# Optimization experiments

Measured on AMD Instinct MI355X. Metric: run time of the kernel, lower is better.

The kernel has to match this reference:

```python
import jax, jax.numpy as jnp
import numpy as np
import math

HIDDEN = 32
N_NODES = 4096
N_EDGES = 8192
FEAT = HIDDEN * 16
# e3nn FullyConnectedTensorProduct instruction order: loop i_in1, i_in2, i_out
PATHS = [(l1, l2, l3) for l1 in range(4) for l2 in range(4) for l3 in range(4)
         if abs(l1 - l2) <= l3 <= l1 + l2 and (l1 + l2 + l3) % 2 == 0]
WEIGHT_NUMEL = len(PATHS) * HIDDEN * HIDDEN  # 23 * 1024 = 23552
_CNT = {l3: sum(1 for p in PATHS if p[2] == l3) for l3 in range(4)}
# path_weight: irrep_normalization='component', path_normalization='element'
PATH_W = {p: math.sqrt((2 * p[2] + 1) / (_CNT[p[2]] * HIDDEN)) for p in PATHS}


def _sh(xp, x, y, z):
    # e3nn-convention real spherical harmonics l=0..3, 'component' normalization.
    # Assumes unit-norm (x,y,z). xp is np or jnp.
    s3, s5, s7, s15 = math.sqrt(3.), math.sqrt(5.), math.sqrt(7.), math.sqrt(15.)
    c58, c38 = math.sqrt(5. / 8.), math.sqrt(3. / 8.)
    comps = [
        xp.ones_like(x),
        s3 * x, s3 * y, s3 * z,
        s5 * s3 * x * z, s5 * s3 * x * y, s5 * (y * y - 0.5 * (x * x + z * z)),
        s5 * s3 * y * z, s5 * (s3 / 2.) * (z * z - x * x),
        s7 * c58 * x * (3. * z * z - x * x), s7 * s15 * x * y * z,
        s7 * c38 * x * (5. * y * y - 1.), s7 * 0.5 * y * (5. * y * y - 3.),
        s7 * c38 * z * (5. * y * y - 1.), s7 * (s15 / 2.) * y * (z * z - x * x),
        s7 * c58 * z * (z * z - 3. * x * x),
    ]
    return xp.stack(comps, axis=-1)


def _wigner_tables():
    # Real-basis unit-Frobenius invariant tensors (e3nn wigner_3j up to sign),
    # computed as Gaunt integrals of the real SH over the sphere (exact quadrature:
    # integrand degree <= 9, Gauss-Legendre x uniform phi).
    nu, nphi = 16, 32
    u, wu = np.polynomial.legendre.leggauss(nu)
    phi = np.arange(nphi) * (2.0 * np.pi / nphi)
    uu = np.repeat(u, nphi)
    ww = np.repeat(wu, nphi) * (2.0 * np.pi / nphi)
    pp = np.tile(phi, nu)
    st = np.sqrt(np.maximum(1.0 - uu * uu, 0.0))
    Y = _sh(np, st * np.cos(pp), st * np.sin(pp), uu)  # [P,16]
    tabs = {}
    for key in set(PATHS):
        l1, l2, l3 = key
        C = np.einsum('p,pi,pj,pk->ijk', ww,
                      Y[:, l1 * l1:(l1 + 1) ** 2],
                      Y[:, l2 * l2:(l2 + 1) ** 2],
                      Y[:, l3 * l3:(l3 + 1) ** 2])
        tabs[key] = (C / np.linalg.norm(C)).astype(np.float32)
    return tabs


W3J = _wigner_tables()


def setup_inputs():
    key = jax.random.key(0)
    k1, k2, k3, k4, k5 = jax.random.split(key, 5)
    return {
        'node_features': jax.random.normal(k1, (N_NODES, FEAT), jnp.float32),
        'edge_index': jax.random.randint(k2, (2, N_EDGES), 0, N_NODES),
        'edge_vectors': jax.random.normal(k3, (N_EDGES, 3), jnp.float32),
        'w_weight': jax.random.uniform(k4, (WEIGHT_NUMEL, 1), jnp.float32, -1.0, 1.0),
        'w_bias': jax.random.uniform(k5, (WEIGHT_NUMEL,), jnp.float32, -1.0, 1.0),
    }


def reference(node_features, edge_index, edge_vectors, w_weight, w_bias):
    src, dst = edge_index[0], edge_index[1]
    N = node_features.shape[0]
    E = edge_vectors.shape[0]
    lengths = jnp.maximum(jnp.linalg.norm(edge_vectors, axis=-1, keepdims=True), 1e-8)
    unit = edge_vectors / lengths
    Y = _sh(jnp, unit[:, 0], unit[:, 1], unit[:, 2])            # [E,16]
    # weight_net: Linear(1, weight_numel)
    W = lengths * w_weight[:, 0][None, :] + w_bias[None, :]     # [E,23552]
    x_src = node_features[src]                                  # [E,512] gather
    acc = [jnp.zeros((E, HIDDEN, 2 * l + 1), node_features.dtype) for l in range(4)]
    for p_idx, (l1, l2, l3) in enumerate(PATHS):
        x1 = x_src[:, HIDDEN * l1 * l1: HIDDEN * (l1 + 1) ** 2].reshape(E, HIDDEN, 2 * l1 + 1)
        y2 = Y[:, l2 * l2:(l2 + 1) ** 2]                        # [E,2l2+1]
        C = jnp.asarray(W3J[(l1, l2, l3)])                      # [2l1+1,2l2+1,2l3+1]
        wp = W[:, p_idx * HIDDEN * HIDDEN:(p_idx + 1) * HIDDEN * HIDDEN].reshape(E, HIDDEN, HIDDEN)
        tmp = jnp.einsum('eui,ej,ijk->euk', x1, y2, C)
        acc[l3] = acc[l3] + PATH_W[(l1, l2, l3)] * jnp.einsum('euk,euw->ewk', tmp, wp)
    messages = jnp.concatenate([a.reshape(E, -1) for a in acc], axis=-1)  # [E,512]
    return jax.ops.segment_sum(messages, dst, num_segments=N)
```

## Files before the change

### kernel.cpp

```cpp
#include <hip/hip_runtime.h>
#include <math.h>

#define N_PATHS 23
#define HIDDEN  32
#define N_NODES 4096
#define N_EDGES 8192
#define FEAT    512
#define BLK     128
#define ZERO_BLOCKS 256

#define WAVE_SYNC() asm volatile("s_waitcnt lgkmcnt(0)" ::: "memory")

typedef __attribute__((ext_vector_type(8)))  short bf16x8;
typedef __attribute__((ext_vector_type(16))) float f32x16;

constexpr int cL1[N_PATHS] = {0,0,0,0, 1,1,1,1,1,1, 2,2,2,2,2,2,2, 3,3,3,3,3,3};
constexpr int cL2[N_PATHS] = {0,1,2,3, 0,1,1,2,2,3, 0,1,1,2,2,3,3, 0,1,2,2,3,3};
constexpr int cCOFF[N_PATHS]= {0,1,10,35,84,93,102,147,192,297,402,427,472,577,602,727,832,1077,1126,1231,1336,1581,1630};
constexpr int cL3P[N_PATHS] = {0,5,13,21, 1,4,7,11,15,19, 2,6,9,10,14,18,22, 3,8,12,16,17,20};
constexpr int cL3S[5] = {0,4,10,17,23};
constexpr int cOFF3[4] = {0,32,128,288};
__device__ const int CNT_L3[4] = {4,6,7,6};
__device__ const int D_L3[N_PATHS] = {0,1,2,3, 1,0,2,1,3,2, 2,1,3,0,2,1,3, 3,2,1,3,0,2};

constexpr int zOff(int G, int pi) {
    int off = 0;
    for (int q = cL3S[G]; q < pi; ++q) off += (2*cL1[cL3P[q]]+1)*(2*G+1);
    return off;
}

__device__ const double GLX8[8] = {
    -0.96028985649753623168, -0.79666647741362673959, -0.52553240991632898582, -0.18343464249564980494,
     0.18343464249564980494,  0.52553240991632898582,  0.79666647741362673959,  0.96028985649753623168};
__device__ const double GLW8[8] = {
     0.10122853629037625915,  0.22238103445337447054,  0.31370664587788728734,  0.36268378337836198297,
     0.36268378337836198297,  0.31370664587788728734,  0.22238103445337447054,  0.10122853629037625915};
__device__ const double COSP16[16] = {
  1.0,                     0.92387953251128675613,  0.70710678118654752440,  0.38268343236508977173,
  0.0,                    -0.38268343236508977173, -0.70710678118654752440, -0.92387953251128675613,
 -1.0,                    -0.92387953251128675613, -0.70710678118654752440, -0.38268343236508977173,
  0.0,                     0.38268343236508977173,  0.70710678118654752440,  0.92387953251128675613};
__device__ const double SINP16[16] = {
  0.0,                     0.38268343236508977173,  0.70710678118654752440,  0.92387953251128675613,
  1.0,                     0.92387953251128675613,  0.70710678118654752440,  0.38268343236508977173,
  0.0,                    -0.38268343236508977173, -0.70710678118654752440, -0.92387953251128675613,
 -1.0,                    -0.92387953251128675613, -0.70710678118654752440, -0.38268343236508977173};

__device__ inline void sh_f64(double x, double y, double z, double* Y) {
    const double s3 = 1.7320508075688772935, s5 = 2.2360679774997896964,
                 s7 = 2.6457513110645905905, s15 = 3.8729833462074168852;
    const double c58 = 0.79056941504209483300, c38 = 0.61237243569579452455;
    Y[0] = 1.0;
    Y[1] = s3*x;  Y[2] = s3*y;  Y[3] = s3*z;
    Y[4] = s5*s3*x*z;  Y[5] = s5*s3*x*y;
    Y[6] = s5*(y*y - 0.5*(x*x + z*z));
    Y[7] = s5*s3*y*z;  Y[8] = s5*(s3/2.0)*(z*z - x*x);
    Y[9] = s7*c58*x*(3.0*z*z - x*x);
    Y[10]= s7*s15*x*y*z;
    Y[11]= s7*c38*x*(5.0*y*y - 1.0);
    Y[12]= s7*0.5*y*(5.0*y*y - 3.0);
    Y[13]= s7*c38*z*(5.0*y*y - 1.0);
    Y[14]= s7*(s15/2.0)*y*(z*z - x*x);
    Y[15]= s7*c58*z*(z*z - 3.0*x*x);
}

__device__ inline void sh_f32(float x, float y, float z, float* Y) {
    const float s3 = 1.73205080757f, s5 = 2.23606797750f, s7 = 2.64575131106f, s15 = 3.87298334621f;
    const float c58 = 0.79056941504f, c38 = 0.61237243570f;
    Y[0] = 1.0f;
    Y[1] = s3*x;  Y[2] = s3*y;  Y[3] = s3*z;
    Y[4] = s15*x*z;  Y[5] = s15*x*y;
    Y[6] = s5*(y*y - 0.5f*(x*x + z*z));
    Y[7] = s15*y*z;  Y[8] = s5*(s3*0.5f)*(z*z - x*x);
    Y[9] = s7*c58*x*(3.0f*z*z - x*x);
    Y[10]= s7*s15*x*y*z;
    Y[11]= s7*c38*x*(5.0f*y*y - 1.0f);
    Y[12]= s7*0.5f*y*(5.0f*y*y - 3.0f);
    Y[13]= s7*c38*z*(5.0f*y*y - 1.0f);
    Y[14]= s7*(s15*0.5f)*y*(z*z - x*x);
    Y[15]= s7*c58*z*(z*z - 3.0f*x*x);
}

__device__ inline unsigned short bf16rne(float x) {
    unsigned int u = __float_as_uint(x);
    unsigned int r = (u + 0x7FFFu + ((u >> 16) & 1u)) >> 16;
    return (unsigned short)r;
}
__device__ inline float bf16f(unsigned short h) {
    return __uint_as_float(((unsigned int)h) << 16);
}

__global__ __launch_bounds__(512) void w3j_setup_kernel(
    const float* __restrict__ ww, const float* __restrict__ wb,
    float* __restrict__ g_w3j,
    unsigned short* __restrict__ Awhi, unsigned short* __restrict__ Awlo,
    unsigned short* __restrict__ Abhi, unsigned short* __restrict__ Ablo,
    float* __restrict__ out) {
    const int t = threadIdx.x;

    if (blockIdx.x >= N_PATHS) {
        const int b = blockIdx.x - N_PATHS;
        float4* o4 = (float4*)(out + (size_t)b * (N_NODES*FEAT/ZERO_BLOCKS));
#pragma unroll
        for (int r = 0; r < 4; ++r)
            o4[t + 512*r] = make_float4(0.f,0.f,0.f,0.f);
        return;
    }

    __shared__ float s_Yq[128][17];
    __shared__ float s_wq[128];
    __shared__ float s_part[256];
    __shared__ float red[256];
    __shared__ float s_scale;

    const int p = blockIdx.x;
    const int l1 = cL1[p], l2 = cL2[p];
    const int l3 = D_L3[p];
    const int d2 = 2*l2+1, d3 = 2*l3+1;
    const int csize = (2*l1+1)*d2*d3;
    const double step = 2.0*3.14159265358979323846/16.0;

#pragma unroll
    for (int r = 0; r < 2; ++r) {
        const int idx = t + 512*r;
        const int w = idx >> 5, u = idx & 31;
        const float vw = ww[p*1024 + u*32 + w];
        const float vb = wb[p*1024 + u*32 + w];
        const unsigned short hw = bf16rne(vw);
        const unsigned short hb = bf16rne(vb);
        const int o = p*1024 + w*32 + u;
        Awhi[o] = hw;  Awlo[o] = bf16rne(vw - bf16f(hw));
        Abhi[o] = hb;  Ablo[o] = bf16rne(vb - bf16f(hb));
    }

    if (t < 128) {
        const int iu = t >> 4, ip = t & 15;
        const double u = GLX8[iu];
        const double st = sqrt(fmax(1.0 - u*u, 0.0));
        double Y[16];
        sh_f64(st*COSP16[ip], st*SINP16[ip], u, Y);
#pragma unroll
        for (int i = 0; i < 16; ++i) s_Yq[t][i] = (float)Y[i];
        s_wq[t] = (float)(GLW8[iu] * step);
    }
    __syncthreads();

    const int entry0 = t >> 2, sub = t & 3;
#pragma unroll
    for (int pass = 0; pass < 2; ++pass) {
        const int entry = entry0 + pass*128;
        float acc = 0.f;
        if (entry < csize) {
            const int i = entry/(d2*d3); const int r = entry - i*(d2*d3);
            const int j = r/d3; const int k = r - j*d3;
            const int ai = l1*l1+i, bi = l2*l2+j, ci = l3*l3+k;
#pragma unroll 4
            for (int it = 0; it < 32; ++it) {
                const int q = it*4 + sub;
                acc = fmaf(s_wq[q] * s_Yq[q][ai] * s_Yq[q][bi], s_Yq[q][ci], acc);
            }
        }
        acc += __shfl_xor(acc, 1);
        acc += __shfl_xor(acc, 2);
        if (sub == 0 && entry < csize) s_part[entry] = acc;
    }
    __syncthreads();

    if (t < 256) { const float v = (t < csize) ? s_part[t] : 0.f; red[t] = v*v; }
    __syncthreads();
    for (int s = 128; s > 0; s >>= 1) {
        if (t < s) red[t] += red[t+s];
        __syncthreads();
    }
    if (t == 0) {
        const float pw = sqrtf((float)(2*l3+1) / ((float)CNT_L3[l3] * (float)HIDDEN));
        s_scale = pw / sqrtf(red[0]);
    }
    __syncthreads();
    if (t < csize) g_w3j[cCOFF[p] + t] = s_part[t] * s_scale;
}

template<int G, int P, int ZOFF>
__device__ __forceinline__ void do_zpath(
    int lane, const float* __restrict__ w3j, const float* sY, float* sz)
{
    constexpr int l1 = cL1[P], l2 = cL2[P];
    constexpr int d1 = 2*l1+1, d2 = 2*l2+1, d3 = 2*G+1;
    constexpr int zc = d1*d3;
#pragma unroll
    for (int base = 0; base < 4*zc; base += 64) {
        const int idx = base + lane;
        if (idx < 4*zc) {
            const int elz = idx / zc;
            const int r = idx - elz*zc;
            const int i = r / d3, k = r - i*d3;
            const float* Cp = w3j + cCOFF[P] + i*(d2*d3) + k;
            const float* Yp = sY + elz*16 + l2*l2;
            float acc = 0.f;
#pragma unroll
            for (int j = 0; j < d2; ++j) acc = fmaf(Yp[j], Cp[j*d3], acc);
            sz[4*ZOFF + elz*zc + r] = acc;
        }
    }
}

template<int G, int P, int ZOFF>
__device__ __forceinline__ void do_path(
    int lane, int el4, int u0, int bvaddr, int avaddr,
    const float (&xr0)[16], const float (&xr1)[16],
    const unsigned short* __restrict__ Awhi, const unsigned short* __restrict__ Awlo,
    const unsigned short* __restrict__ Abhi, const unsigned short* __restrict__ Ablo,
    const float* sz,
    unsigned short* sbh, unsigned short* sbl,
    f32x16 &Cw, f32x16 &Cb)
{
    constexpr int l1 = cL1[P];
    constexpr int d1 = 2*l1+1, d3 = 2*G+1;
    constexpr int zc = d1*d3;
    constexpr int xo = l1*l1;

    const unsigned short* pwh = Awhi + P*1024;
    const unsigned short* pwl = Awlo + P*1024;
    const unsigned short* pbh = Abhi + P*1024;
    const unsigned short* pbl = Ablo + P*1024;
    bf16x8 awh[2], awl[2], abh[2], abl[2];
#pragma unroll
    for (int kc = 0; kc < 2; ++kc) {
        awh[kc] = *(const bf16x8*)(pwh + avaddr + kc*16);
        awl[kc] = *(const bf16x8*)(pwl + avaddr + kc*16);
        abh[kc] = *(const bf16x8*)(pbh + avaddr + kc*16);
        abl[kc] = *(const bf16x8*)(pbl + avaddr + kc*16);
    }

    {
        const float* zr = sz + 4*ZOFF + el4*zc;
        unsigned short* bh = sbh + (el4*d3)*40 + 2*u0;
        unsigned short* bl = sbl + (el4*d3)*40 + 2*u0;
#pragma unroll
        for (int k = 0; k < d3; ++k) {
            float t0 = 0.f, t1 = 0.f;
#pragma unroll
            for (int i = 0; i < d1; ++i) {
                const float zz = zr[i*d3 + k];
                t0 = fmaf(xr0[xo+i], zz, t0);
                t1 = fmaf(xr1[xo+i], zz, t1);
            }
            const unsigned int b0 = __float_as_uint(t0);
            const unsigned int b1 = __float_as_uint(t1);
            const float l0 = t0 - __uint_as_float(b0 & 0xFFFF0000u);
            const float l1f = t1 - __uint_as_float(b1 & 0xFFFF0000u);
            *(unsigned int*)(bh + k*40) = (b0 >> 16) | (b1 & 0xFFFF0000u);
            *(unsigned int*)(bl + k*40) = (__float_as_uint(l0) >> 16) | (__float_as_uint(l1f) & 0xFFFF0000u);
        }
    }
    WAVE_SYNC();

#pragma unroll
    for (int kc = 0; kc < 2; ++kc) {
        const bf16x8 bh = *(const bf16x8*)(sbh + bvaddr + kc*16);
        const bf16x8 bl = *(const bf16x8*)(sbl + bvaddr + kc*16);
        Cw = __builtin_amdgcn_mfma_f32_32x32x16_bf16(awh[kc], bh, Cw, 0, 0, 0);
        Cb = __builtin_amdgcn_mfma_f32_32x32x16_bf16(abh[kc], bh, Cb, 0, 0, 0);
        Cw = __builtin_amdgcn_mfma_f32_32x32x16_bf16(awh[kc], bl, Cw, 0, 0, 0);
        Cb = __builtin_amdgcn_mfma_f32_32x32x16_bf16(abh[kc], bl, Cb, 0, 0, 0);
        Cw = __builtin_amdgcn_mfma_f32_32x32x16_bf16(awl[kc], bh, Cw, 0, 0, 0);
        Cb = __builtin_amdgcn_mfma_f32_32x32x16_bf16(abl[kc], bh, Cb, 0, 0, 0);
    }
    WAVE_SYNC();
}

template<int G>
__device__ __forceinline__ void do_group(
    int lane, int el4, int u0, int bvaddr, int avaddr,
    const float (&xr0)[16], const float (&xr1)[16],
    const float* __restrict__ w3j,
    const unsigned short* __restrict__ Awhi, const unsigned short* __restrict__ Awlo,
    const unsigned short* __restrict__ Abhi, const unsigned short* __restrict__ Ablo,
    const float* sY, float* sz,
    unsigned short* sbh, unsigned short* sbl,
    const float* slen, float* smsg)
{
    constexpr int d3 = 2*G+1;
    constexpr int s = cL3S[G];
    constexpr int n = cL3S[G+1] - cL3S[G];
    f32x16 Cw = (f32x16)(0.f), Cb = (f32x16)(0.f);

    do_zpath<G, cL3P[s+0], zOff(G,s+0)>(lane, w3j, sY, sz);
    do_zpath<G, cL3P[s+1], zOff(G,s+1)>(lane, w3j, sY, sz);
    do_zpath<G, cL3P[s+2], zOff(G,s+2)>(lane, w3j, sY, sz);
    do_zpath<G, cL3P[s+3], zOff(G,s+3)>(lane, w3j, sY, sz);
    if constexpr (n > 4) do_zpath<G, cL3P[s+4], zOff(G,s+4)>(lane, w3j, sY, sz);
    if constexpr (n > 5) do_zpath<G, cL3P[s+5], zOff(G,s+5)>(lane, w3j, sY, sz);
    if constexpr (n > 6) do_zpath<G, cL3P[s+6], zOff(G,s+6)>(lane, w3j, sY, sz);
    WAVE_SYNC();

    do_path<G, cL3P[s+0], zOff(G,s+0)>(lane,el4,u0,bvaddr,avaddr,xr0,xr1,Awhi,Awlo,Abhi,Ablo,sz,sbh,sbl,Cw,Cb);
    do_path<G, cL3P[s+1], zOff(G,s+1)>(lane,el4,u0,bvaddr,avaddr,xr0,xr1,Awhi,Awlo,Abhi,Ablo,sz,sbh,sbl,Cw,Cb);
    do_path<G, cL3P[s+2], zOff(G,s+2)>(lane,el4,u0,bvaddr,avaddr,xr0,xr1,Awhi,Awlo,Abhi,Ablo,sz,sbh,sbl,Cw,Cb);
    do_path<G, cL3P[s+3], zOff(G,s+3)>(lane,el4,u0,bvaddr,avaddr,xr0,xr1,Awhi,Awlo,Abhi,Ablo,sz,sbh,sbl,Cw,Cb);
    if constexpr (n > 4)
        do_path<G, cL3P[s+4], zOff(G,s+4)>(lane,el4,u0,bvaddr,avaddr,xr0,xr1,Awhi,Awlo,Abhi,Ablo,sz,sbh,sbl,Cw,Cb);
    if constexpr (n > 5)
        do_path<G, cL3P[s+5], zOff(G,s+5)>(lane,el4,u0,bvaddr,avaddr,xr0,xr1,Awhi,Awlo,Abhi,Ablo,sz,sbh,sbl,Cw,Cb);
    if constexpr (n > 6)
        do_path<G, cL3P[s+6], zOff(G,s+6)>(lane,el4,u0,bvaddr,avaddr,xr0,xr1,Awhi,Awlo,Abhi,Ablo,sz,sbh,sbl,Cw,Cb);

    const int col = lane & 31;
    if (col < 4*d3) {
        const int elc = col / d3, k = col - elc*d3;
        const float len = slen[elc];
        float* mp = smsg + elc*FEAT + cOFF3[G] + k;
#pragma unroll
        for (int reg = 0; reg < 16; ++reg) {
            const int w = (reg & 3) + 8*(reg >> 2) + 4*(lane >> 5);
            mp[w*d3] = fmaf(len, Cw[reg], Cb[reg]);
        }
    }
}

__global__ __launch_bounds__(BLK) void edge_kernel(
    const float* __restrict__ nf,
    const int*   __restrict__ eidx,
    const float* __restrict__ ev,
    const float* __restrict__ w3j,
    const unsigned short* __restrict__ Awhi,
    const unsigned short* __restrict__ Awlo,
    const unsigned short* __restrict__ Abhi,
    const unsigned short* __restrict__ Ablo,
    float*       __restrict__ out)
{
    __shared__ float s_zp[2][784];
    __shared__ float s_Y[2][64];
    __shared__ float s_len[2][4];
    __shared__ int   s_src[2][4];
    __shared__ int   s_dst[2][4];
    __shared__ __align__(16) unsigned short s_Bhi[2][1280];
    __shared__ __align__(16) unsigned short s_Blo[2][1280];
    __shared__ float s_msg[2][4*FEAT];

    const int t    = threadIdx.x;
    const int wave = t >> 6;
    const int lane = t & 63;
    const int el4  = lane >> 4;
    const int u0   = lane & 15;
    const int e0   = blockIdx.x * 8 + wave*4;
    const int bvaddr = (lane & 31)*40 + (lane >> 5)*8;
    const int avaddr = (lane & 31)*32 + (lane >> 5)*8;

    if (lane < 4) {
        const int e = e0 + lane;
        s_src[wave][lane] = eidx[e];
        s_dst[wave][lane] = eidx[N_EDGES + e];
        const float x = ev[e*3+0], y = ev[e*3+1], z = ev[e*3+2];
        const float len = sqrtf(x*x + y*y + z*z);
        const float lc = fmaxf(len, 1e-8f);
        s_len[wave][lane] = lc;
        float Yl[16];
        sh_f32(x/lc, y/lc, z/lc, Yl);
#pragma unroll
        for (int i = 0; i < 16; ++i) s_Y[wave][lane*16+i] = Yl[i];
    }
    WAVE_SYNC();

    float xr0[16], xr1[16];
    {
        const float* xrow = nf + (size_t)s_src[wave][el4]*FEAT;
        const int ua = 2*u0, ub = 2*u0 + 1;
        xr0[0] = xrow[ua];                 xr1[0] = xrow[ub];
#pragma unroll
        for (int i = 0; i < 3; ++i) { xr0[1+i] = xrow[32 + ua*3 + i];  xr1[1+i] = xrow[32 + ub*3 + i]; }
#pragma unroll
        for (int i = 0; i < 5; ++i) { xr0[4+i] = xrow[128 + ua*5 + i]; xr1[4+i] = xrow[128 + ub*5 + i]; }
#pragma unroll
        for (int i = 0; i < 7; ++i) { xr0[9+i] = xrow[288 + ua*7 + i]; xr1[9+i] = xrow[288 + ub*7 + i]; }
    }

    do_group<0>(lane,el4,u0,bvaddr,avaddr,xr0,xr1,w3j,Awhi,Awlo,Abhi,Ablo,
                s_Y[wave], s_zp[wave], s_Bhi[wave], s_Blo[wave], s_len[wave], s_msg[wave]);
    do_group<1>(lane,el4,u0,bvaddr,avaddr,xr0,xr1,w3j,Awhi,Awlo,Abhi,Ablo,
                s_Y[wave], s_zp[wave], s_Bhi[wave], s_Blo[wave], s_len[wave], s_msg[wave]);
    do_group<2>(lane,el4,u0,bvaddr,avaddr,xr0,xr1,w3j,Awhi,Awlo,Abhi,Ablo,
                s_Y[wave], s_zp[wave], s_Bhi[wave], s_Blo[wave], s_len[wave], s_msg[wave]);
    do_group<3>(lane,el4,u0,bvaddr,avaddr,xr0,xr1,w3j,Awhi,Awlo,Abhi,Ablo,
                s_Y[wave], s_zp[wave], s_Bhi[wave], s_Blo[wave], s_len[wave], s_msg[wave]);
    WAVE_SYNC();

    for (int i = lane; i < 4*FEAT; i += 64) {
        const int elc = i >> 9, m = i & 511;
        atomicAdd(&out[(size_t)s_dst[wave][elc]*FEAT + m], s_msg[wave][i]);
    }
}

extern "C" void kernel_launch(void* const* d_in, const int* in_sizes, int n_in,
                              void* d_out, int out_size, void* d_ws, size_t ws_size,
                              hipStream_t stream) {
    const float* nf   = (const float*)d_in[0];
    const int*   eidx = (const int*)  d_in[1];
    const float* ev   = (const float*)d_in[2];
    const float* ww   = (const float*)d_in[3];
    const float* wb   = (const float*)d_in[4];
    float* out = (float*)d_out;

    float* w3j = (float*)d_ws;
    unsigned short* Awhi = (unsigned short*)((char*)d_ws + 16384);
    unsigned short* Awlo = Awhi + N_PATHS*1024;
    unsigned short* Abhi = Awlo + N_PATHS*1024;
    unsigned short* Ablo = Abhi + N_PATHS*1024;

    w3j_setup_kernel<<<N_PATHS + ZERO_BLOCKS, 512, 0, stream>>>(
        ww, wb, w3j, Awhi, Awlo, Abhi, Ablo, out);
    edge_kernel<<<N_EDGES/8, BLK, 0, stream>>>(nf, eidx, ev, w3j, Awhi, Awlo, Abhi, Ablo, out);
}
```

Before: 122.2 us.

## Replace per-path template unrolling with runtime loops and stage source features in LDS

Swaps the fully template-unrolled per-path code for runtime loops driven by device lookup tables. This should shrink code size and register pressure. Source node features are now loaded coalesced into shared memory in an irrep-transposed layout instead of held in per-thread register arrays. The atomic scatter to the output moves into each l3 group, so the message buffer shrinks to one group. The cost is extra LDS traffic, table lookups, non-constexpr loop bounds inside the rewritten loops, and more LDS per block.

```diff
diff --git a/kernel.cpp b/kernel.cpp
--- a/kernel.cpp
+++ b/kernel.cpp
@@ -14,20 +14,20 @@
 typedef __attribute__((ext_vector_type(8)))  short bf16x8;
 typedef __attribute__((ext_vector_type(16))) float f32x16;
 
-constexpr int cL1[N_PATHS] = {0,0,0,0, 1,1,1,1,1,1, 2,2,2,2,2,2,2, 3,3,3,3,3,3};
-constexpr int cL2[N_PATHS] = {0,1,2,3, 0,1,1,2,2,3, 0,1,1,2,2,3,3, 0,1,2,2,3,3};
-constexpr int cCOFF[N_PATHS]= {0,1,10,35,84,93,102,147,192,297,402,427,472,577,602,727,832,1077,1126,1231,1336,1581,1630};
-constexpr int cL3P[N_PATHS] = {0,5,13,21, 1,4,7,11,15,19, 2,6,9,10,14,18,22, 3,8,12,16,17,20};
 constexpr int cL3S[5] = {0,4,10,17,23};
 constexpr int cOFF3[4] = {0,32,128,288};
 __device__ const int CNT_L3[4] = {4,6,7,6};
-__device__ const int D_L3[N_PATHS] = {0,1,2,3, 1,0,2,1,3,2, 2,1,3,0,2,1,3, 3,2,1,3,0,2};
-
-constexpr int zOff(int G, int pi) {
-    int off = 0;
-    for (int q = cL3S[G]; q < pi; ++q) off += (2*cL1[cL3P[q]]+1)*(2*G+1);
-    return off;
-}
+
+__device__ const int mPATH[N_PATHS] = {0,5,13,21, 1,4,7,11,15,19, 2,6,9,10,14,18,22, 3,8,12,16,17,20};
+__device__ const int mD1  [N_PATHS] = {1,3,5,7, 1,3,3,5,5,7, 1,3,3,5,5,7,7, 1,3,5,5,7,7};
+__device__ const int mXO  [N_PATHS] = {0,1,4,9, 0,1,1,4,4,9, 0,1,1,4,4,9,9, 0,1,4,4,9,9};
+__device__ const int mL2  [N_PATHS] = {0,1,2,3, 1,0,2,1,3,2, 2,1,3,0,2,1,3, 3,2,1,3,0,2};
+__device__ const int mCOFF[N_PATHS] = {0,93,577,1581, 1,84,147,427,727,1231, 10,102,297,402,602,1126,1630, 35,192,472,832,1077,1336};
+__device__ const int mZOFF[N_PATHS] = {0,1,4,9, 0,3,12,21,36,51, 0,5,20,35,60,85,120, 0,7,28,63,98,147};
+__device__ const int pL1[N_PATHS] = {0,0,0,0, 1,1,1,1,1,1, 2,2,2,2,2,2,2, 3,3,3,3,3,3};
+__device__ const int pL2[N_PATHS] = {0,1,2,3, 0,1,1,2,2,3, 0,1,1,2,2,3,3, 0,1,2,2,3,3};
+__device__ const int pCOFF[N_PATHS]= {0,1,10,35,84,93,102,147,192,297,402,427,472,577,602,727,832,1077,1126,1231,1336,1581,1630};
+__device__ const int pD_L3[N_PATHS] = {0,1,2,3, 1,0,2,1,3,2, 2,1,3,0,2,1,3, 3,2,1,3,0,2};
 
 __device__ const double GLX8[8] = {
     -0.96028985649753623168, -0.79666647741362673959, -0.52553240991632898582, -0.18343464249564980494,
@@ -114,8 +114,8 @@
     __shared__ float s_scale;
 
     const int p = blockIdx.x;
-    const int l1 = cL1[p], l2 = cL2[p];
-    const int l3 = D_L3[p];
+    const int l1 = pL1[p], l2 = pL2[p];
+    const int l3 = pD_L3[p];
     const int d2 = 2*l2+1, d3 = 2*l3+1;
     const int csize = (2*l1+1)*d2*d3;
     const double step = 2.0*3.14159265358979323846/16.0;
@@ -177,145 +177,139 @@
         s_scale = pw / sqrtf(red[0]);
     }
     __syncthreads();
-    if (t < csize) g_w3j[cCOFF[p] + t] = s_part[t] * s_scale;
-}
-
-template<int G, int P, int ZOFF>
-__device__ __forceinline__ void do_zpath(
-    int lane, const float* __restrict__ w3j, const float* sY, float* sz)
-{
-    constexpr int l1 = cL1[P], l2 = cL2[P];
-    constexpr int d1 = 2*l1+1, d2 = 2*l2+1, d3 = 2*G+1;
-    constexpr int zc = d1*d3;
-#pragma unroll
-    for (int base = 0; base < 4*zc; base += 64) {
-        const int idx = base + lane;
-        if (idx < 4*zc) {
-            const int elz = idx / zc;
-            const int r = idx - elz*zc;
-            const int i = r / d3, k = r - i*d3;
-            const float* Cp = w3j + cCOFF[P] + i*(d2*d3) + k;
-            const float* Yp = sY + elz*16 + l2*l2;
-            float acc = 0.f;
-#pragma unroll
-            for (int j = 0; j < d2; ++j) acc = fmaf(Yp[j], Cp[j*d3], acc);
-            sz[4*ZOFF + elz*zc + r] = acc;
-        }
-    }
-}
-
-template<int G, int P, int ZOFF>
-__device__ __forceinline__ void do_path(
-    int lane, int el4, int u0, int bvaddr, int avaddr,
-    const float (&xr0)[16], const float (&xr1)[16],
-    const unsigned short* __restrict__ Awhi, const unsigned short* __restrict__ Awlo,
-    const unsigned short* __restrict__ Abhi, const unsigned short* __restrict__ Ablo,
-    const float* sz,
-    unsigned short* sbh, unsigned short* sbl,
-    f32x16 &Cw, f32x16 &Cb)
-{
-    constexpr int l1 = cL1[P];
-    constexpr int d1 = 2*l1+1, d3 = 2*G+1;
-    constexpr int zc = d1*d3;
-    constexpr int xo = l1*l1;
-
-    const unsigned short* pwh = Awhi + P*1024;
-    const unsigned short* pwl = Awlo + P*1024;
-    const unsigned short* pbh = Abhi + P*1024;
-    const unsigned short* pbl = Ablo + P*1024;
-    bf16x8 awh[2], awl[2], abh[2], abl[2];
-#pragma unroll
-    for (int kc = 0; kc < 2; ++kc) {
-        awh[kc] = *(const bf16x8*)(pwh + avaddr + kc*16);
-        awl[kc] = *(const bf16x8*)(pwl + avaddr + kc*16);
-        abh[kc] = *(const bf16x8*)(pbh + avaddr + kc*16);
-        abl[kc] = *(const bf16x8*)(pbl + avaddr + kc*16);
-    }
-
-    {
-        const float* zr = sz + 4*ZOFF + el4*zc;
-        unsigned short* bh = sbh + (el4*d3)*40 + 2*u0;
-        unsigned short* bl = sbl + (el4*d3)*40 + 2*u0;
-#pragma unroll
-        for (int k = 0; k < d3; ++k) {
-            float t0 = 0.f, t1 = 0.f;
-#pragma unroll
-            for (int i = 0; i < d1; ++i) {
-                const float zz = zr[i*d3 + k];
-                t0 = fmaf(xr0[xo+i], zz, t0);
-                t1 = fmaf(xr1[xo+i], zz, t1);
-            }
-            const unsigned int b0 = __float_as_uint(t0);
-            const unsigned int b1 = __float_as_uint(t1);
-            const float l0 = t0 - __uint_as_float(b0 & 0xFFFF0000u);
-            const float l1f = t1 - __uint_as_float(b1 & 0xFFFF0000u);
-            *(unsigned int*)(bh + k*40) = (b0 >> 16) | (b1 & 0xFFFF0000u);
-            *(unsigned int*)(bl + k*40) = (__float_as_uint(l0) >> 16) | (__float_as_uint(l1f) & 0xFFFF0000u);
-        }
-    }
-    WAVE_SYNC();
-
-#pragma unroll
-    for (int kc = 0; kc < 2; ++kc) {
-        const bf16x8 bh = *(const bf16x8*)(sbh + bvaddr + kc*16);
-        const bf16x8 bl = *(const bf16x8*)(sbl + bvaddr + kc*16);
-        Cw = __builtin_amdgcn_mfma_f32_32x32x16_bf16(awh[kc], bh, Cw, 0, 0, 0);
-        Cb = __builtin_amdgcn_mfma_f32_32x32x16_bf16(abh[kc], bh, Cb, 0, 0, 0);
-        Cw = __builtin_amdgcn_mfma_f32_32x32x16_bf16(awh[kc], bl, Cw, 0, 0, 0);
-        Cb = __builtin_amdgcn_mfma_f32_32x32x16_bf16(abh[kc], bl, Cb, 0, 0, 0);
-        Cw = __builtin_amdgcn_mfma_f32_32x32x16_bf16(awl[kc], bh, Cw, 0, 0, 0);
-        Cb = __builtin_amdgcn_mfma_f32_32x32x16_bf16(abl[kc], bh, Cb, 0, 0, 0);
-    }
-    WAVE_SYNC();
+    if (t < csize) g_w3j[pCOFF[p] + t] = s_part[t] * s_scale;
 }
 
 template<int G>
 __device__ __forceinline__ void do_group(
     int lane, int el4, int u0, int bvaddr, int avaddr,
-    const float (&xr0)[16], const float (&xr1)[16],
     const float* __restrict__ w3j,
     const unsigned short* __restrict__ Awhi, const unsigned short* __restrict__ Awlo,
     const unsigned short* __restrict__ Abhi, const unsigned short* __restrict__ Ablo,
-    const float* sY, float* sz,
+    const float* sY, const float* sx, float* sz,
     unsigned short* sbh, unsigned short* sbl,
-    const float* slen, float* smsg)
+    const float* slen, const int* sdst, float* smsg, float* __restrict__ out)
 {
     constexpr int d3 = 2*G+1;
-    constexpr int s = cL3S[G];
-    constexpr int n = cL3S[G+1] - cL3S[G];
+    constexpr int s0 = cL3S[G];
+    constexpr int n  = cL3S[G+1] - cL3S[G];
     f32x16 Cw = (f32x16)(0.f), Cb = (f32x16)(0.f);
 
-    do_zpath<G, cL3P[s+0], zOff(G,s+0)>(lane, w3j, sY, sz);
-    do_zpath<G, cL3P[s+1], zOff(G,s+1)>(lane, w3j, sY, sz);
-    do_zpath<G, cL3P[s+2], zOff(G,s+2)>(lane, w3j, sY, sz);
-    do_zpath<G, cL3P[s+3], zOff(G,s+3)>(lane, w3j, sY, sz);
-    if constexpr (n > 4) do_zpath<G, cL3P[s+4], zOff(G,s+4)>(lane, w3j, sY, sz);
-    if constexpr (n > 5) do_zpath<G, cL3P[s+5], zOff(G,s+5)>(lane, w3j, sY, sz);
-    if constexpr (n > 6) do_zpath<G, cL3P[s+6], zOff(G,s+6)>(lane, w3j, sY, sz);
+#pragma unroll 1
+    for (int j = 0; j < n; ++j) {
+        const int s   = s0 + j;
+        const int l2  = mL2[s];
+        const int d2  = 2*l2 + 1;
+        const int d1  = mD1[s];
+        const int zc  = d1*d3;
+        const int cof = mCOFF[s];
+        const int zo4 = 4*mZOFF[s];
+        if (lane < zc) {
+            const int i = lane / d3;
+            const int k = lane - i*d3;
+            const float* Cp = w3j + cof + i*(d2*d3) + k;
+#pragma unroll
+            for (int el = 0; el < 4; ++el) {
+                const float* Yp = sY + el*16 + l2*l2;
+                float acc = 0.f;
+                for (int jj = 0; jj < d2; ++jj) acc = fmaf(Yp[jj], Cp[jj*d3], acc);
+                sz[zo4 + el*zc + lane] = acc;
+            }
+        }
+    }
     WAVE_SYNC();
 
-    do_path<G, cL3P[s+0], zOff(G,s+0)>(lane,el4,u0,bvaddr,avaddr,xr0,xr1,Awhi,Awlo,Abhi,Ablo,sz,sbh,sbl,Cw,Cb);
-    do_path<G, cL3P[s+1], zOff(G,s+1)>(lane,el4,u0,bvaddr,avaddr,xr0,xr1,Awhi,Awlo,Abhi,Ablo,sz,sbh,sbl,Cw,Cb);
-    do_path<G, cL3P[s+2], zOff(G,s+2)>(lane,el4,u0,bvaddr,avaddr,xr0,xr1,Awhi,Awlo,Abhi,Ablo,sz,sbh,sbl,Cw,Cb);
-    do_path<G, cL3P[s+3], zOff(G,s+3)>(lane,el4,u0,bvaddr,avaddr,xr0,xr1,Awhi,Awlo,Abhi,Ablo,sz,sbh,sbl,Cw,Cb);
-    if constexpr (n > 4)
-        do_path<G, cL3P[s+4], zOff(G,s+4)>(lane,el4,u0,bvaddr,avaddr,xr0,xr1,Awhi,Awlo,Abhi,Ablo,sz,sbh,sbl,Cw,Cb);
-    if constexpr (n > 5)
-        do_path<G, cL3P[s+5], zOff(G,s+5)>(lane,el4,u0,bvaddr,avaddr,xr0,xr1,Awhi,Awlo,Abhi,Ablo,sz,sbh,sbl,Cw,Cb);
-    if constexpr (n > 6)
-        do_path<G, cL3P[s+6], zOff(G,s+6)>(lane,el4,u0,bvaddr,avaddr,xr0,xr1,Awhi,Awlo,Abhi,Ablo,sz,sbh,sbl,Cw,Cb);
-
+#pragma unroll 1
+    for (int j = 0; j < n; ++j) {
+        const int s    = s0 + j;
+        const int Poff = mPATH[s] << 10;
+        const int d1   = mD1[s];
+        const int xo   = mXO[s];
+        const int zc   = d1*d3;
+        const int zo4  = 4*mZOFF[s];
+
+        bf16x8 awh[2], awl[2], abh[2], abl[2];
+#pragma unroll
+        for (int kc = 0; kc < 2; ++kc) {
+            awh[kc] = *(const bf16x8*)(Awhi + Poff + avaddr + kc*16);
+            awl[kc] = *(const bf16x8*)(Awlo + Poff + avaddr + kc*16);
+            abh[kc] = *(const bf16x8*)(Abhi + Poff + avaddr + kc*16);
+            abl[kc] = *(const bf16x8*)(Ablo + Poff + avaddr + kc*16);
+        }
+
+        {
+            const float* zr = sz + zo4 + el4*zc;
+            const float* xp = sx + el4*512 + xo*32 + 2*u0;
+            float tk0[d3], tk1[d3];
+#pragma unroll
+            for (int k = 0; k < d3; ++k) { tk0[k] = 0.f; tk1[k] = 0.f; }
+            float2 xv = *(const float2*)(xp);
+            float zrow[d3];
+#pragma unroll
+            for (int k = 0; k < d3; ++k) zrow[k] = zr[k];
+            for (int i = 0; i < d1; ++i) {
+                const int ip = (i+1 < d1) ? (i+1) : i;
+                const float2 xn = *(const float2*)(xp + ip*32);
+                float zn[d3];
+#pragma unroll
+                for (int k = 0; k < d3; ++k) zn[k] = zr[ip*d3 + k];
+#pragma unroll
+                for (int k = 0; k < d3; ++k) {
+                    tk0[k] = fmaf(xv.x, zrow[k], tk0[k]);
+                    tk1[k] = fmaf(xv.y, zrow[k], tk1[k]);
+                }
+                xv = xn;
+#pragma unroll
+                for (int k = 0; k < d3; ++k) zrow[k] = zn[k];
+            }
+            unsigned short* bh = sbh + (el4*d3)*40 + 2*u0;
+            unsigned short* bl = sbl + (el4*d3)*40 + 2*u0;
+#pragma unroll
+            for (int k = 0; k < d3; ++k) {
+                const unsigned int b0 = __float_as_uint(tk0[k]);
+                const unsigned int b1 = __float_as_uint(tk1[k]);
+                const float l0  = tk0[k] - __uint_as_float(b0 & 0xFFFF0000u);
+                const float l1f = tk1[k] - __uint_as_float(b1 & 0xFFFF0000u);
+                *(unsigned int*)(bh + k*40) = (b0 >> 16) | (b1 & 0xFFFF0000u);
+                *(unsigned int*)(bl + k*40) = (__float_as_uint(l0) >> 16) | (__float_as_uint(l1f) & 0xFFFF0000u);
+            }
+        }
+        WAVE_SYNC();
+
+#pragma unroll
+        for (int kc = 0; kc < 2; ++kc) {
+            const bf16x8 bh = *(const bf16x8*)(sbh + bvaddr + kc*16);
+            const bf16x8 bl = *(const bf16x8*)(sbl + bvaddr + kc*16);
+            Cw = __builtin_amdgcn_mfma_f32_32x32x16_bf16(awh[kc], bh, Cw, 0, 0, 0);
+            Cb = __builtin_amdgcn_mfma_f32_32x32x16_bf16(abh[kc], bh, Cb, 0, 0, 0);
+            Cw = __builtin_amdgcn_mfma_f32_32x32x16_bf16(awh[kc], bl, Cw, 0, 0, 0);
+            Cb = __builtin_amdgcn_mfma_f32_32x32x16_bf16(abh[kc], bl, Cb, 0, 0, 0);
+            Cw = __builtin_amdgcn_mfma_f32_32x32x16_bf16(awl[kc], bh, Cw, 0, 0, 0);
+            Cb = __builtin_amdgcn_mfma_f32_32x32x16_bf16(abl[kc], bh, Cb, 0, 0, 0);
+        }
+        WAVE_SYNC();
+    }
+
+    constexpr int gsz = 32*d3;
     const int col = lane & 31;
     if (col < 4*d3) {
         const int elc = col / d3, k = col - elc*d3;
         const float len = slen[elc];
-        float* mp = smsg + elc*FEAT + cOFF3[G] + k;
+        float* mp = smsg + elc*gsz + k;
 #pragma unroll
         for (int reg = 0; reg < 16; ++reg) {
             const int w = (reg & 3) + 8*(reg >> 2) + 4*(lane >> 5);
             mp[w*d3] = fmaf(len, Cw[reg], Cb[reg]);
         }
     }
+    WAVE_SYNC();
+
+    for (int i2 = lane; i2 < 4*gsz; i2 += 64) {
+        const int el = i2 / gsz;
+        const int m  = i2 - el*gsz;
+        atomicAdd(&out[(size_t)sdst[el]*FEAT + cOFF3[G] + m], smsg[el*gsz + m]);
+    }
+    WAVE_SYNC();
 }
 
 __global__ __launch_bounds__(BLK) void edge_kernel(
@@ -336,7 +330,8 @@
     __shared__ int   s_dst[2][4];
     __shared__ __align__(16) unsigned short s_Bhi[2][1280];
     __shared__ __align__(16) unsigned short s_Blo[2][1280];
-    __shared__ float s_msg[2][4*FEAT];
+    __shared__ float s_msg[2][896];
+    __shared__ float s_x[2][2048];
 
     const int t    = threadIdx.x;
     const int wave = t >> 6;
@@ -362,33 +357,46 @@
     }
     WAVE_SYNC();
 
-    float xr0[16], xr1[16];
     {
-        const float* xrow = nf + (size_t)s_src[wave][el4]*FEAT;
-        const int ua = 2*u0, ub = 2*u0 + 1;
-        xr0[0] = xrow[ua];                 xr1[0] = xrow[ub];
-#pragma unroll
-        for (int i = 0; i < 3; ++i) { xr0[1+i] = xrow[32 + ua*3 + i];  xr1[1+i] = xrow[32 + ub*3 + i]; }
-#pragma unroll
-        for (int i = 0; i < 5; ++i) { xr0[4+i] = xrow[128 + ua*5 + i]; xr1[4+i] = xrow[128 + ub*5 + i]; }
-#pragma unroll
-        for (int i = 0; i < 7; ++i) { xr0[9+i] = xrow[288 + ua*7 + i]; xr1[9+i] = xrow[288 + ub*7 + i]; }
-    }
-
-    do_group<0>(lane,el4,u0,bvaddr,avaddr,xr0,xr1,w3j,Awhi,Awlo,Abhi,Ablo,
-                s_Y[wave], s_zp[wave], s_Bhi[wave], s_Blo[wave], s_len[wave], s_msg[wave]);
-    do_group<1>(lane,el4,u0,bvaddr,avaddr,xr0,xr1,w3j,Awhi,Awlo,Abhi,Ablo,
-                s_Y[wave], s_zp[wave], s_Bhi[wave], s_Blo[wave], s_len[wave], s_msg[wave]);
-    do_group<2>(lane,el4,u0,bvaddr,avaddr,xr0,xr1,w3j,Awhi,Awlo,Abhi,Ablo,
-                s_Y[wave], s_zp[wave], s_Bhi[wave], s_Blo[wave], s_len[wave], s_msg[wave]);
-    do_group<3>(lane,el4,u0,bvaddr,avaddr,xr0,xr1,w3j,Awhi,Awlo,Abhi,Ablo,
-                s_Y[wave], s_zp[wave], s_Bhi[wave], s_Blo[wave], s_len[wave], s_msg[wave]);
+        float* sx = s_x[wave];
+#pragma unroll
+        for (int idx = lane; idx < 4*32; idx += 64) {
+            const int el = idx >> 5, m = idx & 31;
+            sx[el*512 + m] = nf[(size_t)s_src[wave][el]*FEAT + m];
+        }
+#pragma unroll
+        for (int idx = lane; idx < 4*96; idx += 64) {
+            const int el = idx/96, m = idx - el*96;
+            const int u = m/3, i = m - 3*u;
+            sx[el*512 + (1+i)*32 + u] = nf[(size_t)s_src[wave][el]*FEAT + 32 + m];
+        }
+#pragma unroll
+        for (int idx = lane; idx < 4*160; idx += 64) {
+            const int el = idx/160, m = idx - el*160;
+            const int u = m/5, i = m - 5*u;
+            sx[el*512 + (4+i)*32 + u] = nf[(size_t)s_src[wave][el]*FEAT + 128 + m];
+        }
+#pragma unroll
+        for (int idx = lane; idx < 4*224; idx += 64) {
+            const int el = idx/224, m = idx - el*224;
+            const int u = m/7, i = m - 7*u;
+            sx[el*512 + (9+i)*32 + u] = nf[(size_t)s_src[wave][el]*FEAT + 288 + m];
+        }
+    }
     WAVE_SYNC();
 
-    for (int i = lane; i < 4*FEAT; i += 64) {
-        const int elc = i >> 9, m = i & 511;
-        atomicAdd(&out[(size_t)s_dst[wave][elc]*FEAT + m], s_msg[wave][i]);
-    }
+    do_group<0>(lane,el4,u0,bvaddr,avaddr,w3j,Awhi,Awlo,Abhi,Ablo,
+                s_Y[wave], s_x[wave], s_zp[wave], s_Bhi[wave], s_Blo[wave],
+                s_len[wave], s_dst[wave], s_msg[wave], out);
+    do_group<1>(lane,el4,u0,bvaddr,avaddr,w3j,Awhi,Awlo,Abhi,Ablo,
+                s_Y[wave], s_x[wave], s_zp[wave], s_Bhi[wave], s_Blo[wave],
+                s_len[wave], s_dst[wave], s_msg[wave], out);
+    do_group<2>(lane,el4,u0,bvaddr,avaddr,w3j,Awhi,Awlo,Abhi,Ablo,
+                s_Y[wave], s_x[wave], s_zp[wave], s_Bhi[wave], s_Blo[wave],
+                s_len[wave], s_dst[wave], s_msg[wave], out);
+    do_group<3>(lane,el4,u0,bvaddr,avaddr,w3j,Awhi,Awlo,Abhi,Ablo,
+                s_Y[wave], s_x[wave], s_zp[wave], s_Bhi[wave], s_Blo[wave],
+                s_len[wave], s_dst[wave], s_msg[wave], out);
 }
 
 extern "C" void kernel_launch(void* const* d_in, const int* in_sizes, int n_in,
```

Result: slower. 161.1 us (+31.8%).
